# Optimization experiments

Hardware: AMD Instinct MI355X
Metric: run time of the kernel (lower is better)

The kernel has to match this reference:

```python
import jax, jax.numpy as jnp
import numpy as np

B, S, T = 8, 128, 24          # batch, src_len, max_len (enc_len = 2*S)
V, E, H = 32000, 512, 512     # vocab, embed_dim, hidden_dim
D = 3 * H + E                 # pointer-head feature dim = 2*dec_hid + emb + enc_hid


def setup_inputs() -> dict:
    key = jax.random.key(0)
    ks = jax.random.split(key, 25)
    def u(k, shape, scale):
        return jax.random.uniform(k, shape, jnp.float32, -scale, scale)
    s_h = 1.0 / np.sqrt(H).astype(np.float32)
    s_d = 1.0 / np.sqrt(D).astype(np.float32)
    s_2h = 1.0 / np.sqrt(2 * H).astype(np.float32)
    return {
        'pre_seq': jax.random.randint(ks[0], (B, S), 0, V),
        'post_seq': jax.random.randint(ks[1], (B, S), 0, V),
        'trg': jax.random.randint(ks[2], (B, T), 0, V),
        'emb': jax.random.normal(ks[3], (V, E), jnp.float32) * 0.02,
        'Wih_pre': u(ks[4], (3 * H, E), s_h), 'Whh_pre': u(ks[5], (3 * H, H), s_h),
        'bih_pre': u(ks[6], (3 * H,), s_h), 'bhh_pre': u(ks[7], (3 * H,), s_h),
        'Wih_post': u(ks[8], (3 * H, E), s_h), 'Whh_post': u(ks[9], (3 * H, H), s_h),
        'bih_post': u(ks[10], (3 * H,), s_h), 'bhh_post': u(ks[11], (3 * H,), s_h),
        'fc_enc_W': u(ks[12], (H, 2 * H), s_2h), 'fc_enc_b': u(ks[13], (H,), s_2h),
        'attn_W': u(ks[14], (H, 2 * H), s_2h), 'attn_b': u(ks[15], (H,), s_2h),
        'attn_v': u(ks[16], (1, H), s_h),
        'Wih_dec': u(ks[17], (3 * H, H + E), s_h), 'Whh_dec': u(ks[18], (3 * H, H), s_h),
        'bih_dec': u(ks[19], (3 * H,), s_h), 'bhh_dec': u(ks[20], (3 * H,), s_h),
        'fc_hid_W': u(ks[21], (D, D), s_d), 'fc_hid_b': u(ks[22], (D,), s_d),
        'fc_out_W': u(ks[23], (1, D), s_d), 'fc_out_b': u(ks[24], (1,), s_d),
    }


def gru_cell(x, h, Wih, Whh, bih, bhh):
    # torch GRU gate order: reset, update, new
    gi = x @ Wih.T + bih
    gh = h @ Whh.T + bhh
    ir, iz, inn = jnp.split(gi, 3, axis=-1)
    hr, hz, hn = jnp.split(gh, 3, axis=-1)
    r = jax.nn.sigmoid(ir + hr)
    z = jax.nn.sigmoid(iz + hz)
    n = jnp.tanh(inn + r * hn)
    return (1.0 - z) * n + z * h


def run_gru(x_seq, Wih, Whh, bih, bhh):
    # x_seq: [B, L, E] -> outputs [B, L, H], last hidden [B, H]
    h0 = jnp.zeros((x_seq.shape[0], Whh.shape[1]), x_seq.dtype)
    def step(h, x):
        h2 = gru_cell(x, h, Wih, Whh, bih, bhh)
        return h2, h2
    h_last, ys = jax.lax.scan(step, h0, jnp.swapaxes(x_seq, 0, 1))
    return jnp.swapaxes(ys, 0, 1), h_last


def reference(pre_seq, post_seq, trg, emb,
              Wih_pre, Whh_pre, bih_pre, bhh_pre,
              Wih_post, Whh_post, bih_post, bhh_post,
              fc_enc_W, fc_enc_b, attn_W, attn_b, attn_v,
              Wih_dec, Whh_dec, bih_dec, bhh_dec,
              fc_hid_W, fc_hid_b, fc_out_W, fc_out_b):
    bsz, src_len = pre_seq.shape
    # ---- Encoder (dropout in eval mode = identity) ----
    pre_out, pre_h = run_gru(emb[pre_seq], Wih_pre, Whh_pre, bih_pre, bhh_pre)
    post_out, post_h = run_gru(emb[post_seq], Wih_post, Whh_post, bih_post, bhh_post)
    enc_out = jnp.concatenate([pre_out, post_out], axis=1)          # [B, 2S, H]
    hidden = jnp.tanh(jnp.concatenate([pre_h, post_h], axis=-1) @ fc_enc_W.T + fc_enc_b)
    # ---- Attention: split attn_W into hidden- and encoder- parts (cat order: hidden, enc) ----
    W_hid, W_enc = attn_W[:, :H], attn_W[:, H:]
    enc_proj = jnp.einsum('blh,dh->bld', enc_out, W_enc) + attn_b   # step-invariant [B, L, H]
    L = enc_out.shape[1]
    # decoder input tokens: pre_seq[:, -1] then trg[:, :-1] (always teacher forced)
    tokens = jnp.concatenate([pre_seq[:, -1:], trg[:, :-1]], axis=1)  # [B, T]

    def dec_step(h, tok):
        e = emb[tok]                                                # [B, E]
        energy = jnp.tanh(enc_proj + (h @ W_hid.T)[:, None, :])     # [B, L, H]
        scores = jnp.einsum('blh,h->bl', energy, attn_v[0])
        a = jax.nn.softmax(scores, axis=1)                          # [B, L]
        weighted = jnp.einsum('bl,blh->bh', a, enc_out)             # [B, H]
        h2 = gru_cell(jnp.concatenate([e, weighted], axis=-1), h,
                      Wih_dec, Whh_dec, bih_dec, bhh_dec)           # [B, H]
        feats = jnp.concatenate([
            enc_out,
            jnp.broadcast_to(weighted[:, None, :], (bsz, L, H)),
            jnp.broadcast_to(h2[:, None, :], (bsz, L, H)),
            jnp.broadcast_to(e[:, None, :], (bsz, L, E)),
        ], axis=-1)                                                 # [B, L, 3H+E]
        hid = feats @ fc_hid_W.T + fc_hid_b                         # [B, L, D]
        logits = (hid @ fc_out_W.T + fc_out_b)[..., 0]              # [B, L]
        return h2, logits

    _, ys = jax.lax.scan(dec_step, hidden, tokens.T)                # [T, B, L]
    outs = jnp.swapaxes(ys, 0, 1)                                   # [B, T, L]
    return outs[:, :, :src_len], outs[:, :, src_len:]
```

## Files before the change

kernel.cpp:

```cpp
#include <hip/hip_runtime.h>
#include <cstdint>

#define B_ 8
#define S_ 128
#define T_ 24
#define E_ 512
#define H_ 512
#define H3_ 1536
#define L_ 256
#define D_ 2048

typedef unsigned long long u64;

__device__ __forceinline__ float fsig(float x) { return 1.0f / (1.0f + __expf(-x)); }
__device__ __forceinline__ float ftanh(float x) { return 1.0f - 2.0f / (1.0f + __expf(2.0f * x)); }
__device__ __forceinline__ float dot4(float4 a, float4 b) {
    return a.x * b.x + a.y * b.y + a.z * b.z + a.w * b.w;
}

__device__ __forceinline__ u64 cohLoadU64(const u64* p) {
    return __hip_atomic_load((u64*)p, __ATOMIC_RELAXED, __HIP_MEMORY_SCOPE_AGENT);
}
__device__ __forceinline__ void cohStoreU64(u64* p, u64 v) {
    __hip_atomic_store(p, v, __ATOMIC_RELAXED, __HIP_MEMORY_SCOPE_AGENT);
}
__device__ __forceinline__ float2 asF2(u64 v) { union { u64 u; float2 f; } x; x.u = v; return x.f; }
__device__ __forceinline__ u64 packF2(float v, float tag) { union { float2 f; u64 u; } x; x.f = make_float2(v, tag); return x.u; }

__global__ void k_init(const int* __restrict__ pre, const int* __restrict__ post,
                       const int* __restrict__ trg,
                       int* __restrict__ idxPre, int* __restrict__ idxPost,
                       int* __restrict__ idxTok, float* __restrict__ wEff) {
    int tid = blockIdx.x * 256 + threadIdx.x;
    if (tid < 1024) {
        int s = tid >> 3, b = tid & 7;
        idxPre[tid]  = pre[b * S_ + s];
        idxPost[tid] = post[b * S_ + s];
    }
    if (tid < T_ * B_) {
        int t = tid >> 3, b = tid & 7;
        idxTok[tid] = (t == 0) ? pre[b * S_ + (S_ - 1)] : trg[b * T_ + (t - 1)];
    }
    wEff[tid] = 0.f;
}

__global__ void k_clear(u64* __restrict__ p, int n) {
    int i = blockIdx.x * 256 + threadIdx.x;
    int stride = gridDim.x * 256;
    for (; i < n; i += stride) p[i] = 0ull;
}

__global__ __launch_bounds__(256) void k_gemm(
    const float* __restrict__ A, const int* __restrict__ Aidx, int lda,
    const float* __restrict__ Bm, int ldb,
    const float* __restrict__ bias, float* __restrict__ C,
    int N, int K) {
    __shared__ float As[16][68];
    __shared__ float Bs[16][68];
    const int m0 = blockIdx.x * 64, n0 = blockIdx.y * 64;
    const int tid = threadIdx.x;
    const int tm = tid >> 2;
    const int tk = (tid & 3) << 2;
    const int tx = tid & 15, ty = tid >> 4;
    const int am = m0 + tm;
    const float* Arow = A + (size_t)(Aidx ? Aidx[am] : am) * lda;
    const float* Brow = Bm + (size_t)(n0 + tm) * ldb;
    float acc[4][4] = {};
    for (int k0 = 0; k0 < K; k0 += 16) {
        float4 av = *(const float4*)(Arow + k0 + tk);
        float4 bv = *(const float4*)(Brow + k0 + tk);
        __syncthreads();
        As[tk][tm] = av.x; As[tk + 1][tm] = av.y; As[tk + 2][tm] = av.z; As[tk + 3][tm] = av.w;
        Bs[tk][tm] = bv.x; Bs[tk + 1][tm] = bv.y; Bs[tk + 2][tm] = bv.z; Bs[tk + 3][tm] = bv.w;
        __syncthreads();
#pragma unroll
        for (int k = 0; k < 16; ++k) {
            float4 a4 = *(const float4*)(&As[k][ty << 2]);
            float4 b4 = *(const float4*)(&Bs[k][tx << 2]);
            float ar[4] = {a4.x, a4.y, a4.z, a4.w};
            float br[4] = {b4.x, b4.y, b4.z, b4.w};
#pragma unroll
            for (int i = 0; i < 4; ++i)
#pragma unroll
                for (int j = 0; j < 4; ++j) acc[i][j] += ar[i] * br[j];
        }
    }
    float4 bb = bias ? *(const float4*)(bias + n0 + (tx << 2)) : make_float4(0.f, 0.f, 0.f, 0.f);
#pragma unroll
    for (int i = 0; i < 4; ++i) {
        int m = m0 + (ty << 2) + i;
        float4 o;
        o.x = acc[i][0] + bb.x; o.y = acc[i][1] + bb.y;
        o.z = acc[i][2] + bb.z; o.w = acc[i][3] + bb.w;
        *(float4*)(C + (size_t)m * N + n0 + (tx << 2)) = o;
    }
}

__global__ void k_weff(const float* __restrict__ fcW, const float* __restrict__ fcB,
                       const float* __restrict__ voW, const float* __restrict__ voB,
                       float* __restrict__ wEff, float* __restrict__ bEff) {
    __shared__ float red[256];
    int bx = blockIdx.x;
    if (bx < 128) {
        int cblk = bx & 7, q = bx >> 3;
        int col = cblk * 256 + threadIdx.x;
        int j0 = q * 128;
        float acc = 0.f;
        for (int j = j0; j < j0 + 128; ++j) acc += voW[j] * fcW[(size_t)j * D_ + col];
        atomicAdd(wEff + col, acc);
    } else {
        float p = 0.f;
        for (int j = threadIdx.x; j < D_; j += 256) p += voW[j] * fcB[j];
        red[threadIdx.x] = p;
        __syncthreads();
        for (int s = 128; s > 0; s >>= 1) {
            if (threadIdx.x < s) red[threadIdx.x] += red[threadIdx.x + s];
            __syncthreads();
        }
        if (threadIdx.x == 0) bEff[0] = red[0] + voB[0];
    }
}

__global__ __launch_bounds__(512, 2) void k_encoder(
    const float* __restrict__ giPre, const float* __restrict__ giPost,
    const float* __restrict__ WhhPre, const float* __restrict__ WhhPost,
    const float* __restrict__ bhhPre, const float* __restrict__ bhhPost,
    float* __restrict__ encOut, u64* __restrict__ encEx) {
    const int bx = blockIdx.x;
    const int chain = bx >> 4;
    const int p = bx & 15;
    const int gr = chain >> 3, b = chain & 7;
    const int kb = p << 5;
    const int tid = threadIdx.x;
    const int c = tid >> 4, l = tid & 15;
    const int j = kb + c;
    const float* gi  = gr ? giPost : giPre;
    const float* Whh = gr ? WhhPost : WhhPre;
    const float* bhh = gr ? bhhPost : bhhPre;
    u64* ex0 = encEx + chain * 512;

    __shared__ float hS[576];

    float wr[32], wz[32], wn[32];
    {
        const float* r0 = Whh + (size_t)j * 512 + l * 32;
        const float* r1 = r0 + 512 * 512;
        const float* r2 = r1 + 512 * 512;
#pragma unroll
        for (int m = 0; m < 32; ++m) { wr[m] = r0[m]; wz[m] = r1[m]; wn[m] = r2[m]; }
    }
    const float bh0 = bhh[j], bh1 = bhh[512 + j], bh2 = bhh[1024 + j];

    for (int t = 0; t < S_; ++t) {
        float g0 = 0.f, g1 = 0.f, g2 = 0.f;
        if (l == 0) {
            size_t gb = ((size_t)(t << 3) + b) * H3_;
            g0 = gi[gb + j]; g1 = gi[gb + 512 + j]; g2 = gi[gb + 1024 + j];
        }
        if (t == 0) {
            hS[(tid >> 5) * 36 + (tid & 31)] = 0.f;
        } else {
            const float tag = (float)t;
            const u64* src = ex0 + (t & 1) * 8192;
            float v;
            for (;;) {
                float2 f = asF2(cohLoadU64(src + tid));
                if (f.y == tag) { v = f.x; break; }
                __builtin_amdgcn_s_sleep(1);
            }
            hS[(tid >> 5) * 36 + (tid & 31)] = v;
        }
        __syncthreads();
        const float* hseg = hS + l * 36;
        float a0 = 0.f, a1 = 0.f, a2 = 0.f;
#pragma unroll
        for (int m = 0; m < 32; ++m) {
            float hv = hseg[m];
            a0 += wr[m] * hv; a1 += wz[m] * hv; a2 += wn[m] * hv;
        }
#pragma unroll
        for (int off = 8; off; off >>= 1) {
            a0 += __shfl_xor(a0, off, 16);
            a1 += __shfl_xor(a1, off, 16);
            a2 += __shfl_xor(a2, off, 16);
        }
        if (l == 0) {
            float r = fsig(g0 + a0 + bh0);
            float z = fsig(g1 + a1 + bh1);
            float n = ftanh(g2 + r * (a2 + bh2));
            float h2 = (1.f - z) * n + z * hS[p * 36 + c];
            cohStoreU64(ex0 + ((t + 1) & 1) * 8192 + j, packF2(h2, (float)(t + 1)));
            encOut[(((size_t)(b << 8) + (gr << 7) + t) << 9) + j] = h2;
        }
        __syncthreads();
    }
}

__global__ void k_fcenc(const float* __restrict__ encOut, const float* __restrict__ W,
                        const float* __restrict__ bias, float* __restrict__ h) {
    int o = blockIdx.x * 256 + threadIdx.x;
    int b = o >> 9, j = o & 511;
    const float4* w4 = (const float4*)(W + (size_t)j * 1024);
    const float4* pre4 = (const float4*)(encOut + (((size_t)(b << 8) + 127) << 9));
    const float4* post4 = (const float4*)(encOut + (((size_t)(b << 8) + 255) << 9));
    float acc = bias[j];
    for (int k = 0; k < 128; ++k) acc += dot4(w4[k], pre4[k]);
    for (int k = 0; k < 128; ++k) acc += dot4(w4[128 + k], post4[k]);
    h[o] = ftanh(acc);
}

__global__ void k_encdot(const float* __restrict__ encOut, const float* __restrict__ wEff,
                         float* __restrict__ encDot) {
    int wid = threadIdx.x >> 6, lane = threadIdx.x & 63;
    int gw = blockIdx.x * 4 + wid;
    for (int o = gw; o < 2048; o += 128) {
        const float* row = encOut + ((size_t)o << 9);
        float s = 0.f;
        for (int k = lane; k < 512; k += 64) s += row[k] * wEff[k];
        for (int off = 32; off; off >>= 1) s += __shfl_down(s, off);
        if (lane == 0) encDot[o] = s;
    }
}

__global__ void k_edot4(const float* __restrict__ emb, const int* __restrict__ idxTok,
                        const float* __restrict__ wEff, float* __restrict__ eDot4) {
    int o = blockIdx.x;
    int lane = threadIdx.x;
    const float* row = emb + (size_t)idxTok[o] * E_;
    const float* w = wEff + 1536;
    float s = 0.f;
    for (int k = lane; k < 512; k += 64) s += row[k] * w[k];
    for (int off = 32; off; off >>= 1) s += __shfl_down(s, off);
    if (lane == 0) eDot4[o] = s;
}

__global__ __launch_bounds__(512, 2) void k_decoder(
    const float* __restrict__ encOut, const float* __restrict__ encProj,
    const float* __restrict__ attnW, const float* __restrict__ attnV,
    const float* __restrict__ WihDec, const float* __restrict__ WhhDec,
    const float* __restrict__ bhhDec, const float* __restrict__ giE,
    const float* __restrict__ wEff, const float* __restrict__ hBuf,
    u64* __restrict__ hEx, u64* __restrict__ hpEx,
    u64* __restrict__ scEx, u64* __restrict__ wtEx,
    float* __restrict__ cpart) {
    const int tid = threadIdx.x;
    const int bx = blockIdx.x;
    __shared__ float hL[4096];
    __shared__ float xL[4096];
    __shared__ float mS[1408];

    if (bx < 32) {
        const int g = bx;
        const int s = tid >> 5, kq = tid & 31;
        const int j = (g << 4) + s;
        float wr[16], wz[16], wn[16], vr[16], vz[16], vn[16];
#pragma unroll
        for (int m = 0; m < 16; ++m) {
            int k = kq + 32 * m;
            wr[m] = WhhDec[(size_t)j * 512 + k];
            wz[m] = WhhDec[(size_t)(512 + j) * 512 + k];
            wn[m] = WhhDec[(size_t)(1024 + j) * 512 + k];
            vr[m] = WihDec[(size_t)j * 1024 + 512 + k];
            vz[m] = WihDec[(size_t)(512 + j) * 1024 + 512 + k];
            vn[m] = WihDec[(size_t)(1024 + j) * 1024 + 512 + k];
        }
        if (tid < 48) mS[1152 + tid] = bhhDec[(tid >> 4) * 512 + (g << 4) + (tid & 15)];
        __syncthreads();
        for (int t = 0; t < T_; ++t) {
            if (t == 0) {
#pragma unroll
                for (int i = 0; i < 8; ++i) hL[tid + 512 * i] = hBuf[tid + 512 * i];
            } else {
                const float tagh = (float)t;
                const u64* src = hEx + (t & 1) * 4096;
                float v[8];
                for (;;) {
                    u64 rr[8];
#pragma unroll
                    for (int i = 0; i < 8; ++i) rr[i] = cohLoadU64(src + tid + 512 * i);
                    bool ok = true;
#pragma unroll
                    for (int i = 0; i < 8; ++i) { float2 f = asF2(rr[i]); v[i] = f.x; ok &= (f.y == tagh); }
                    if (ok) break;
                    __builtin_amdgcn_s_sleep(1);
                }
#pragma unroll
                for (int i = 0; i < 8; ++i) hL[tid + 512 * i] = v[i];
            }
            __syncthreads();
            for (int b = 0; b < 8; ++b) {
                const float* hb = hL + (b << 9);
                float ar = 0.f, az = 0.f, an = 0.f;
#pragma unroll
                for (int m = 0; m < 16; ++m) {
                    float hv = hb[kq + 32 * m];
                    ar += wr[m] * hv; az += wz[m] * hv; an += wn[m] * hv;
                }
#pragma unroll
                for (int off = 16; off; off >>= 1) {
                    ar += __shfl_xor(ar, off); az += __shfl_xor(az, off); an += __shfl_xor(an, off);
                }
                if (kq == 0) {
                    mS[s * 8 + b]       = ar + mS[1152 + s];
                    mS[128 + s * 8 + b] = az + mS[1168 + s];
                    mS[256 + s * 8 + b] = an + mS[1184 + s];
                }
            }
            if (tid < 384) {
                int b = tid / 48, idx = tid % 48, g3 = idx >> 4, ss = idx & 15;
                mS[768 + g3 * 128 + ss * 8 + b] =
                    giE[((size_t)(t << 3) + b) * H3_ + g3 * 512 + (g << 4) + ss];
            }
            {
                const float tagw = (float)(t + 1);
                const u64* src = wtEx + (t & 1) * 4096;
                float v[8];
                for (;;) {
                    u64 rr[8];
#pragma unroll
                    for (int i = 0; i < 8; ++i) rr[i] = cohLoadU64(src + tid + 512 * i);
                    bool ok = true;
#pragma unroll
                    for (int i = 0; i < 8; ++i) { float2 f = asF2(rr[i]); v[i] = f.x; ok &= (f.y == tagw); }
                    if (ok) break;
                    __builtin_amdgcn_s_sleep(1);
                }
#pragma unroll
                for (int i = 0; i < 8; ++i) xL[tid + 512 * i] = v[i];
            }
            __syncthreads();
            for (int b = 0; b < 8; ++b) {
                const float* wb = xL + (b << 9);
                float ar = 0.f, az = 0.f, an = 0.f;
#pragma unroll
                for (int m = 0; m < 16; ++m) {
                    float wv = wb[kq + 32 * m];
                    ar += vr[m] * wv; az += vz[m] * wv; an += vn[m] * wv;
                }
#pragma unroll
                for (int off = 16; off; off >>= 1) {
                    ar += __shfl_xor(ar, off); az += __shfl_xor(az, off); an += __shfl_xor(an, off);
                }
                if (kq == 0) {
                    mS[384 + s * 8 + b] = ar;
                    mS[512 + s * 8 + b] = az;
                    mS[640 + s * 8 + b] = an;
                }
            }
            __syncthreads();
            if (tid < 128) {
                int ss = tid >> 3, b = tid & 7;
                int jj = (g << 4) + ss;
                int o = ss * 8 + b;
                float ghr = mS[o], ghz = mS[128 + o], ghn = mS[256 + o];
                float gir = mS[384 + o] + mS[768 + o];
                float giz = mS[512 + o] + mS[896 + o];
                float gin = mS[640 + o] + mS[1024 + o];
                float r = fsig(gir + ghr), z = fsig(giz + ghz);
                float n = ftanh(gin + r * ghn);
                float h2 = (1.f - z) * n + z * hL[(b << 9) + jj];
                cohStoreU64(hEx + ((t + 1) & 1) * 4096 + (b << 9) + jj, packF2(h2, (float)(t + 1)));
                mS[1200 + o] = h2 * wEff[1024 + jj];
            }
            __syncthreads();
            if (tid < 8) {
                float pc = 0.f;
#pragma unroll
                for (int q = 0; q < 16; ++q) pc += mS[1200 + q * 8 + tid];
                cpart[(tid * T_ + t) * 48 + g] = pc;
            }
            __syncthreads();
        }
    } else if (bx < 48) {
        const int w = bx - 32;
        const int s = tid >> 5, kq = tid & 31;
        const int r0 = (w << 5) + s, r1 = r0 + 16;
        float wa[16], wb[16];
#pragma unroll
        for (int m = 0; m < 16; ++m) {
            int k = kq + 32 * m;
            wa[m] = attnW[(size_t)r0 * 1024 + k];
            wb[m] = attnW[(size_t)r1 * 1024 + k];
        }
        for (int t = 0; t < T_; ++t) {
            if (t == 0) {
#pragma unroll
                for (int i = 0; i < 8; ++i) hL[tid + 512 * i] = hBuf[tid + 512 * i];
            } else {
                const float tagh = (float)t;
                const u64* src = hEx + (t & 1) * 4096;
                float v[8];
                for (;;) {
                    u64 rr[8];
#pragma unroll
                    for (int i = 0; i < 8; ++i) rr[i] = cohLoadU64(src + tid + 512 * i);
                    bool ok = true;
#pragma unroll
                    for (int i = 0; i < 8; ++i) { float2 f = asF2(rr[i]); v[i] = f.x; ok &= (f.y == tagh); }
                    if (ok) break;
                    __builtin_amdgcn_s_sleep(1);
                }
#pragma unroll
                for (int i = 0; i < 8; ++i) hL[tid + 512 * i] = v[i];
            }
            __syncthreads();
            const float tago = (float)(t + 1);
            u64* dst = hpEx + (t & 1) * 4096;
            for (int b = 0; b < 8; ++b) {
                const float* hb = hL + (b << 9);
                float aa = 0.f, ab = 0.f;
#pragma unroll
                for (int m = 0; m < 16; ++m) {
                    float hv = hb[kq + 32 * m];
                    aa += wa[m] * hv; ab += wb[m] * hv;
                }
#pragma unroll
                for (int off = 16; off; off >>= 1) { aa += __shfl_xor(aa, off); ab += __shfl_xor(ab, off); }
                if (kq == 0) {
                    cohStoreU64(dst + (b << 9) + r0, packF2(aa, tago));
                    cohStoreU64(dst + (b << 9) + r1, packF2(ab, tago));
                }
            }
            __syncthreads();
        }
    } else if (bx < 112) {
        const int id = bx - 48;
        const int b = id >> 3, lq = id & 7;
        const int kq = tid & 63, lg = tid >> 6;
        for (int t = 0; t < T_; ++t) {
            const float tagi = (float)(t + 1);
            {
                const u64* src = hpEx + (t & 1) * 4096 + (b << 9);
                float2 f;
                for (;;) {
                    f = asF2(cohLoadU64(src + tid));
                    if (f.y == tagi) break;
                    __builtin_amdgcn_s_sleep(1);
                }
                hL[tid] = f.x;
            }
            __syncthreads();
            u64* dst = scEx + (t & 1) * 2048 + (b << 8);
#pragma unroll
            for (int i = 0; i < 4; ++i) {
                int l = (lq << 5) + lg + (i << 3);
                const float* ep = encProj + (((size_t)(b << 8) + l) << 9);
                float sc = 0.f;
#pragma unroll
                for (int m = 0; m < 8; ++m) {
                    int k = kq + (m << 6);
                    sc += attnV[k] * ftanh(ep[k] + hL[k]);
                }
#pragma unroll
                for (int off = 32; off; off >>= 1) sc += __shfl_xor(sc, off);
                if (kq == 0) cohStoreU64(dst + l, packF2(sc, tagi));
            }
            __syncthreads();
        }
    } else if (bx < 176) {
        const int id = bx - 112;
        const int b = id >> 3, cq = id & 7;
        const int c = tid & 63, lg = tid >> 6;
        for (int t = 0; t < T_; ++t) {
            const float tagi = (float)(t + 1);
            if (tid < 256) {
                const u64* src = scEx + (t & 1) * 2048 + (b << 8);
                float2 f;
                for (;;) {
                    f = asF2(cohLoadU64(src + tid));
                    if (f.y == tagi) break;
                    __builtin_amdgcn_s_sleep(1);
                }
                mS[tid] = f.x;
            }
            __syncthreads();
            if (tid < 256) mS[256 + tid] = mS[tid];
            __syncthreads();
            for (int st = 128; st; st >>= 1) {
                if (tid < st) mS[256 + tid] = fmaxf(mS[256 + tid], mS[256 + tid + st]);
                __syncthreads();
            }
            float mx = mS[256];
            __syncthreads();
            if (tid < 256) { float ex = __expf(mS[tid] - mx); mS[tid] = ex; mS[256 + tid] = ex; }
            __syncthreads();
            for (int st = 128; st; st >>= 1) {
                if (tid < st) mS[256 + tid] += mS[256 + tid + st];
                __syncthreads();
            }
            float inv = 1.f / mS[256];
            float acc = 0.f;
            const float* eb = encOut + (((size_t)(b << 8)) << 9) + (cq << 6) + c;
#pragma unroll
            for (int m = 0; m < 32; ++m) {
                int l = lg + (m << 3);
                acc += mS[l] * eb[(size_t)l << 9];
            }
            mS[512 + lg * 64 + c] = acc;
            __syncthreads();
            if (tid < 64) {
                float wv = 0.f;
#pragma unroll
                for (int q = 0; q < 8; ++q) wv += mS[512 + q * 64 + tid];
                wv *= inv;
                cohStoreU64(wtEx + (t & 1) * 4096 + (b << 9) + (cq << 6) + tid, packF2(wv, tagi));
                mS[1024 + tid] = wv * wEff[512 + (cq << 6) + tid];
            }
            __syncthreads();
            if (tid == 0) {
                float pc = 0.f;
                for (int q = 0; q < 64; ++q) pc += mS[1024 + q];
                cpart[(b * T_ + t) * 48 + 32 + cq] = pc;
            }
            __syncthreads();
        }
    }
}

__global__ void k_csum(const float* __restrict__ cpart, const float* __restrict__ eDot4,
                       const float* __restrict__ bEff, float* __restrict__ cBuf) {
    int tid = threadIdx.x;
    if (tid < 192) {
        int b = tid / 24, t = tid % 24;
        float acc = eDot4[t * 8 + b] + bEff[0];
        const float* p = cpart + (b * T_ + t) * 48;
#pragma unroll
        for (int k = 0; k < 40; ++k) acc += p[k];
        cBuf[b * T_ + t] = acc;
    }
}

__global__ void k_final(const float* __restrict__ encDot, const float* __restrict__ c,
                        float* __restrict__ out) {
    int idx = blockIdx.x * 256 + threadIdx.x;
    const int half = B_ * T_ * S_;
    int w = idx < half ? idx : idx - half;
    int b = w / (T_ * S_);
    int r = w % (T_ * S_);
    int t = r / S_, sidx = r % S_;
    int l = (idx < half) ? sidx : (S_ + sidx);
    out[idx] = encDot[b * L_ + l] + c[b * T_ + t];
}

extern "C" void kernel_launch(void* const* d_in, const int* in_sizes, int n_in,
                              void* d_out, int out_size, void* d_ws, size_t ws_size,
                              hipStream_t stream) {
    const int* pre = (const int*)d_in[0];
    const int* post = (const int*)d_in[1];
    const int* trg = (const int*)d_in[2];
    const float* emb = (const float*)d_in[3];
    const float* WihPre = (const float*)d_in[4];
    const float* WhhPre = (const float*)d_in[5];
    const float* bihPre = (const float*)d_in[6];
    const float* bhhPre = (const float*)d_in[7];
    const float* WihPost = (const float*)d_in[8];
    const float* WhhPost = (const float*)d_in[9];
    const float* bihPost = (const float*)d_in[10];
    const float* bhhPost = (const float*)d_in[11];
    const float* fcEncW = (const float*)d_in[12];
    const float* fcEncB = (const float*)d_in[13];
    const float* attnW = (const float*)d_in[14];
    const float* attnB = (const float*)d_in[15];
    const float* attnV = (const float*)d_in[16];
    const float* WihDec = (const float*)d_in[17];
    const float* WhhDec = (const float*)d_in[18];
    const float* bihDec = (const float*)d_in[19];
    const float* bhhDec = (const float*)d_in[20];
    const float* fcHidW = (const float*)d_in[21];
    const float* fcHidB = (const float*)d_in[22];
    const float* fcOutW = (const float*)d_in[23];
    const float* fcOutB = (const float*)d_in[24];
    float* outp = (float*)d_out;

    float* base = (float*)d_ws;
    size_t off = 0;
    auto alloc = [&](size_t n) {
        float* p = base + off;
        off += (n + 63) & ~(size_t)63;
        return p;
    };
    float* giPre = alloc(1024 * 1536);
    float* giPost = alloc(1024 * 1536);
    float* giE = alloc(192 * 1536);
    float* encOut = alloc(8 * 256 * 512);
    float* encProj = alloc(8 * 256 * 512);
    float* wEff = alloc(2048);
    float* bEff = alloc(64);
    float* encDot = alloc(2048);
    float* eDot4 = alloc(256);
    float* hBuf = alloc(4096);
    float* cBuf = alloc(256);
    float* encExF = alloc(32768);
    float* hExF = alloc(16384);
    float* hpExF = alloc(16384);
    float* scExF = alloc(8192);
    float* wtExF = alloc(16384);
    float* cpart = alloc(8 * 24 * 48);
    int* idxPre = (int*)alloc(1024);
    int* idxPost = (int*)alloc(1024);
    int* idxTok = (int*)alloc(256);

    k_init<<<8, 256, 0, stream>>>(pre, post, trg, idxPre, idxPost, idxTok, wEff);
    k_clear<<<512, 256, 0, stream>>>((u64*)encExF, 45056);
    k_weff<<<129, 256, 0, stream>>>(fcHidW, fcHidB, fcOutW, fcOutB, wEff, bEff);
    k_gemm<<<dim3(16, 24), 256, 0, stream>>>(emb, idxPre, 512, WihPre, 512, bihPre, giPre, 1536, 512);
    k_gemm<<<dim3(16, 24), 256, 0, stream>>>(emb, idxPost, 512, WihPost, 512, bihPost, giPost, 1536, 512);
    k_gemm<<<dim3(3, 24), 256, 0, stream>>>(emb, idxTok, 512, WihDec, 1024, bihDec, giE, 1536, 512);
    k_encoder<<<256, 512, 0, stream>>>(giPre, giPost, WhhPre, WhhPost, bhhPre, bhhPost,
                                       encOut, (u64*)encExF);
    k_gemm<<<dim3(32, 8), 256, 0, stream>>>(encOut, nullptr, 512, attnW + 512, 1024, attnB, encProj, 512, 512);
    k_fcenc<<<16, 256, 0, stream>>>(encOut, fcEncW, fcEncB, hBuf);
    k_encdot<<<32, 256, 0, stream>>>(encOut, wEff, encDot);
    k_edot4<<<192, 64, 0, stream>>>(emb, idxTok, wEff, eDot4);
    k_decoder<<<176, 512, 0, stream>>>(encOut, encProj, attnW, attnV, WihDec, WhhDec, bhhDec,
                                       giE, wEff, hBuf, (u64*)hExF, (u64*)hpExF,
                                       (u64*)scExF, (u64*)wtExF, cpart);
    k_csum<<<1, 256, 0, stream>>>(cpart, eDot4, bEff, cBuf);
    k_final<<<192, 256, 0, stream>>>(encDot, cBuf, outp);
}
```

Before: 1.023 ms.

## Fuse encoder input projection into recurrence and merge auxiliary kernels

Drops the separate pre/post input-projection GEMMs and has each encoder block hold both Wih and Whh slices in registers, computing the input gate contribution per step from gathered embeddings. The small setup kernels (init, clear, weff, gemms, fc_enc) are merged into a boot kernel and a multi-role mid kernel, and encdot/edot4 become extra blocks of the decoder. The decoder is also reorganised: it precomputes hidden attention projections into a larger exchange buffer and uses wave-level shuffle reductions for the softmax. The goal is fewer launches and less GEMM time off the critical path, at the cost of doubled register pressure and extra per-step work in the serial encoder loop.

```diff
diff --git a/kernel.cpp b/kernel.cpp
--- a/kernel.cpp
+++ b/kernel.cpp
@@ -27,37 +27,33 @@
 __device__ __forceinline__ float2 asF2(u64 v) { union { u64 u; float2 f; } x; x.u = v; return x.f; }
 __device__ __forceinline__ u64 packF2(float v, float tag) { union { float2 f; u64 u; } x; x.f = make_float2(v, tag); return x.u; }
 
-__global__ void k_init(const int* __restrict__ pre, const int* __restrict__ post,
+__global__ void k_boot(const int* __restrict__ pre, const int* __restrict__ post,
                        const int* __restrict__ trg,
                        int* __restrict__ idxPre, int* __restrict__ idxPost,
-                       int* __restrict__ idxTok, float* __restrict__ wEff) {
-    int tid = blockIdx.x * 256 + threadIdx.x;
-    if (tid < 1024) {
-        int s = tid >> 3, b = tid & 7;
-        idxPre[tid]  = pre[b * S_ + s];
-        idxPost[tid] = post[b * S_ + s];
-    }
-    if (tid < T_ * B_) {
-        int t = tid >> 3, b = tid & 7;
-        idxTok[tid] = (t == 0) ? pre[b * S_ + (S_ - 1)] : trg[b * T_ + (t - 1)];
-    }
-    wEff[tid] = 0.f;
-}
-
-__global__ void k_clear(u64* __restrict__ p, int n) {
-    int i = blockIdx.x * 256 + threadIdx.x;
-    int stride = gridDim.x * 256;
-    for (; i < n; i += stride) p[i] = 0ull;
-}
-
-__global__ __launch_bounds__(256) void k_gemm(
+                       int* __restrict__ idxTok, float* __restrict__ wEff,
+                       u64* __restrict__ clr, int n) {
+    int gtid = blockIdx.x * 256 + threadIdx.x;
+    for (int i = gtid; i < n; i += gridDim.x * 256) clr[i] = 0ull;
+    if (gtid < 1024) {
+        int s = gtid >> 3, b = gtid & 7;
+        idxPre[gtid]  = pre[b * S_ + s];
+        idxPost[gtid] = post[b * S_ + s];
+    }
+    if (gtid < T_ * B_) {
+        int t = gtid >> 3, b = gtid & 7;
+        idxTok[gtid] = (t == 0) ? pre[b * S_ + (S_ - 1)] : trg[b * T_ + (t - 1)];
+    }
+    if (gtid < 2048) wEff[gtid] = 0.f;
+}
+
+__device__ void gemm_body(
     const float* __restrict__ A, const int* __restrict__ Aidx, int lda,
     const float* __restrict__ Bm, int ldb,
     const float* __restrict__ bias, float* __restrict__ C,
-    int N, int K) {
+    int N, int K, int gbx, int gby) {
     __shared__ float As[16][68];
     __shared__ float Bs[16][68];
-    const int m0 = blockIdx.x * 64, n0 = blockIdx.y * 64;
+    const int m0 = gbx * 64, n0 = gby * 64;
     const int tid = threadIdx.x;
     const int tm = tid >> 2;
     const int tk = (tid & 3) << 2;
@@ -96,33 +92,61 @@
     }
 }
 
-__global__ void k_weff(const float* __restrict__ fcW, const float* __restrict__ fcB,
-                       const float* __restrict__ voW, const float* __restrict__ voB,
-                       float* __restrict__ wEff, float* __restrict__ bEff) {
-    __shared__ float red[256];
-    int bx = blockIdx.x;
-    if (bx < 128) {
-        int cblk = bx & 7, q = bx >> 3;
-        int col = cblk * 256 + threadIdx.x;
-        int j0 = q * 128;
-        float acc = 0.f;
-        for (int j = j0; j < j0 + 128; ++j) acc += voW[j] * fcW[(size_t)j * D_ + col];
-        atomicAdd(wEff + col, acc);
+__global__ __launch_bounds__(256) void k_mid(
+    const float* __restrict__ emb, const int* __restrict__ idxTok,
+    const float* __restrict__ WihDec, const float* __restrict__ bihDec, float* __restrict__ giE,
+    const float* __restrict__ encOut, const float* __restrict__ attnW,
+    const float* __restrict__ attnB, float* __restrict__ encProj,
+    const float* __restrict__ fcHidW, const float* __restrict__ fcHidB,
+    const float* __restrict__ fcOutW, const float* __restrict__ fcOutB,
+    float* __restrict__ wEff, float* __restrict__ bEff,
+    const float* __restrict__ fcEncW, const float* __restrict__ fcEncB,
+    float* __restrict__ hBuf) {
+    const int bx = blockIdx.x;
+    const int tid = threadIdx.x;
+    if (bx < 72) {
+        gemm_body(emb, idxTok, 512, WihDec, 1024, bihDec, giE, 1536, 512, bx % 3, bx / 3);
+    } else if (bx < 328) {
+        int r = bx - 72;
+        gemm_body(encOut, nullptr, 512, attnW + 512, 1024, attnB, encProj, 512, 512, r & 31, r >> 5);
+    } else if (bx < 457) {
+        __shared__ float red[256];
+        int wb = bx - 328;
+        if (wb < 128) {
+            int cblk = wb & 7, q = wb >> 3;
+            int col = cblk * 256 + tid;
+            int j0 = q * 128;
+            float acc = 0.f;
+            for (int j = j0; j < j0 + 128; ++j) acc += fcOutW[j] * fcHidW[(size_t)j * D_ + col];
+            atomicAdd(wEff + col, acc);
+        } else {
+            float p = 0.f;
+            for (int j = tid; j < D_; j += 256) p += fcOutW[j] * fcHidB[j];
+            red[tid] = p;
+            __syncthreads();
+            for (int s = 128; s > 0; s >>= 1) {
+                if (tid < s) red[tid] += red[tid + s];
+                __syncthreads();
+            }
+            if (tid == 0) bEff[0] = red[0] + fcOutB[0];
+        }
     } else {
-        float p = 0.f;
-        for (int j = threadIdx.x; j < D_; j += 256) p += voW[j] * fcB[j];
-        red[threadIdx.x] = p;
-        __syncthreads();
-        for (int s = 128; s > 0; s >>= 1) {
-            if (threadIdx.x < s) red[threadIdx.x] += red[threadIdx.x + s];
-            __syncthreads();
-        }
-        if (threadIdx.x == 0) bEff[0] = red[0] + voB[0];
+        int o = (bx - 457) * 256 + tid;
+        int b = o >> 9, j = o & 511;
+        const float4* w4 = (const float4*)(fcEncW + (size_t)j * 1024);
+        const float4* pre4 = (const float4*)(encOut + (((size_t)(b << 8) + 127) << 9));
+        const float4* post4 = (const float4*)(encOut + (((size_t)(b << 8) + 255) << 9));
+        float acc = fcEncB[j];
+        for (int k = 0; k < 128; ++k) acc += dot4(w4[k], pre4[k]);
+        for (int k = 0; k < 128; ++k) acc += dot4(w4[128 + k], post4[k]);
+        hBuf[o] = ftanh(acc);
     }
 }
 
 __global__ __launch_bounds__(512, 2) void k_encoder(
-    const float* __restrict__ giPre, const float* __restrict__ giPost,
+    const float* __restrict__ emb, const int* __restrict__ idxPre, const int* __restrict__ idxPost,
+    const float* __restrict__ WihPre, const float* __restrict__ WihPost,
+    const float* __restrict__ bihPre, const float* __restrict__ bihPost,
     const float* __restrict__ WhhPre, const float* __restrict__ WhhPost,
     const float* __restrict__ bhhPre, const float* __restrict__ bhhPost,
     float* __restrict__ encOut, u64* __restrict__ encEx) {
@@ -134,29 +158,38 @@
     const int tid = threadIdx.x;
     const int c = tid >> 4, l = tid & 15;
     const int j = kb + c;
-    const float* gi  = gr ? giPost : giPre;
+    const float* Wih = gr ? WihPost : WihPre;
+    const float* bih = gr ? bihPost : bihPre;
     const float* Whh = gr ? WhhPost : WhhPre;
     const float* bhh = gr ? bhhPost : bhhPre;
+    const int* idx = gr ? idxPost : idxPre;
     u64* ex0 = encEx + chain * 512;
 
     __shared__ float hS[576];
-
-    float wr[32], wz[32], wn[32];
+    __shared__ float eS[576];
+
+    float wr[32], wz[32], wn[32], ur[32], uz[32], un[32];
     {
         const float* r0 = Whh + (size_t)j * 512 + l * 32;
         const float* r1 = r0 + 512 * 512;
         const float* r2 = r1 + 512 * 512;
-#pragma unroll
-        for (int m = 0; m < 32; ++m) { wr[m] = r0[m]; wz[m] = r1[m]; wn[m] = r2[m]; }
-    }
-    const float bh0 = bhh[j], bh1 = bhh[512 + j], bh2 = bhh[1024 + j];
+        const float* u0 = Wih + (size_t)j * 512 + l * 32;
+        const float* u1 = u0 + 512 * 512;
+        const float* u2 = u1 + 512 * 512;
+#pragma unroll
+        for (int m = 0; m < 32; ++m) {
+            wr[m] = r0[m]; wz[m] = r1[m]; wn[m] = r2[m];
+            ur[m] = u0[m]; uz[m] = u1[m]; un[m] = u2[m];
+        }
+    }
+    const float b0 = bih[j] + bhh[j];
+    const float b1 = bih[512 + j] + bhh[512 + j];
+    const float bi2 = bih[1024 + j];
+    const float bh2 = bhh[1024 + j];
 
     for (int t = 0; t < S_; ++t) {
-        float g0 = 0.f, g1 = 0.f, g2 = 0.f;
-        if (l == 0) {
-            size_t gb = ((size_t)(t << 3) + b) * H3_;
-            g0 = gi[gb + j]; g1 = gi[gb + 512 + j]; g2 = gi[gb + 1024 + j];
-        }
+        int tok = idx[t * 8 + b];
+        float ev = emb[(size_t)tok * 512 + tid];
         if (t == 0) {
             hS[(tid >> 5) * 36 + (tid & 31)] = 0.f;
         } else {
@@ -170,68 +203,36 @@
             }
             hS[(tid >> 5) * 36 + (tid & 31)] = v;
         }
+        eS[(tid >> 5) * 36 + (tid & 31)] = ev;
         __syncthreads();
         const float* hseg = hS + l * 36;
-        float a0 = 0.f, a1 = 0.f, a2 = 0.f;
+        const float* eseg = eS + l * 36;
+        float a0 = 0.f, a1 = 0.f, a2h = 0.f, a2i = 0.f;
 #pragma unroll
         for (int m = 0; m < 32; ++m) {
-            float hv = hseg[m];
-            a0 += wr[m] * hv; a1 += wz[m] * hv; a2 += wn[m] * hv;
+            float hv = hseg[m], evv = eseg[m];
+            a0 += wr[m] * hv + ur[m] * evv;
+            a1 += wz[m] * hv + uz[m] * evv;
+            a2h += wn[m] * hv;
+            a2i += un[m] * evv;
         }
 #pragma unroll
         for (int off = 8; off; off >>= 1) {
             a0 += __shfl_xor(a0, off, 16);
             a1 += __shfl_xor(a1, off, 16);
-            a2 += __shfl_xor(a2, off, 16);
+            a2h += __shfl_xor(a2h, off, 16);
+            a2i += __shfl_xor(a2i, off, 16);
         }
         if (l == 0) {
-            float r = fsig(g0 + a0 + bh0);
-            float z = fsig(g1 + a1 + bh1);
-            float n = ftanh(g2 + r * (a2 + bh2));
+            float r = fsig(a0 + b0);
+            float z = fsig(a1 + b1);
+            float n = ftanh(a2i + bi2 + r * (a2h + bh2));
             float h2 = (1.f - z) * n + z * hS[p * 36 + c];
             cohStoreU64(ex0 + ((t + 1) & 1) * 8192 + j, packF2(h2, (float)(t + 1)));
             encOut[(((size_t)(b << 8) + (gr << 7) + t) << 9) + j] = h2;
         }
         __syncthreads();
     }
-}
-
-__global__ void k_fcenc(const float* __restrict__ encOut, const float* __restrict__ W,
-                        const float* __restrict__ bias, float* __restrict__ h) {
-    int o = blockIdx.x * 256 + threadIdx.x;
-    int b = o >> 9, j = o & 511;
-    const float4* w4 = (const float4*)(W + (size_t)j * 1024);
-    const float4* pre4 = (const float4*)(encOut + (((size_t)(b << 8) + 127) << 9));
-    const float4* post4 = (const float4*)(encOut + (((size_t)(b << 8) + 255) << 9));
-    float acc = bias[j];
-    for (int k = 0; k < 128; ++k) acc += dot4(w4[k], pre4[k]);
-    for (int k = 0; k < 128; ++k) acc += dot4(w4[128 + k], post4[k]);
-    h[o] = ftanh(acc);
-}
-
-__global__ void k_encdot(const float* __restrict__ encOut, const float* __restrict__ wEff,
-                         float* __restrict__ encDot) {
-    int wid = threadIdx.x >> 6, lane = threadIdx.x & 63;
-    int gw = blockIdx.x * 4 + wid;
-    for (int o = gw; o < 2048; o += 128) {
-        const float* row = encOut + ((size_t)o << 9);
-        float s = 0.f;
-        for (int k = lane; k < 512; k += 64) s += row[k] * wEff[k];
-        for (int off = 32; off; off >>= 1) s += __shfl_down(s, off);
-        if (lane == 0) encDot[o] = s;
-    }
-}
-
-__global__ void k_edot4(const float* __restrict__ emb, const int* __restrict__ idxTok,
-                        const float* __restrict__ wEff, float* __restrict__ eDot4) {
-    int o = blockIdx.x;
-    int lane = threadIdx.x;
-    const float* row = emb + (size_t)idxTok[o] * E_;
-    const float* w = wEff + 1536;
-    float s = 0.f;
-    for (int k = lane; k < 512; k += 64) s += row[k] * w[k];
-    for (int off = 32; off; off >>= 1) s += __shfl_down(s, off);
-    if (lane == 0) eDot4[o] = s;
 }
 
 __global__ __launch_bounds__(512, 2) void k_decoder(
@@ -240,20 +241,19 @@
     const float* __restrict__ WihDec, const float* __restrict__ WhhDec,
     const float* __restrict__ bhhDec, const float* __restrict__ giE,
     const float* __restrict__ wEff, const float* __restrict__ hBuf,
-    u64* __restrict__ hEx, u64* __restrict__ hpEx,
+    const float* __restrict__ emb, const int* __restrict__ idxTok,
+    u64* __restrict__ hEx, u64* __restrict__ hpP,
     u64* __restrict__ scEx, u64* __restrict__ wtEx,
-    float* __restrict__ cpart) {
+    float* __restrict__ cpart, float* __restrict__ encDot, float* __restrict__ eDot4) {
     const int tid = threadIdx.x;
     const int bx = blockIdx.x;
-    __shared__ float hL[4096];
-    __shared__ float xL[4096];
-    __shared__ float mS[1408];
+    __shared__ float shm[9664];
 
     if (bx < 32) {
         const int g = bx;
         const int s = tid >> 5, kq = tid & 31;
         const int j = (g << 4) + s;
-        float wr[16], wz[16], wn[16], vr[16], vz[16], vn[16];
+        float wr[16], wz[16], wn[16], vr[16], vz[16], vn[16], ap[16];
 #pragma unroll
         for (int m = 0; m < 16; ++m) {
             int k = kq + 32 * m;
@@ -263,22 +263,38 @@
             vr[m] = WihDec[(size_t)j * 1024 + 512 + k];
             vz[m] = WihDec[(size_t)(512 + j) * 1024 + 512 + k];
             vn[m] = WihDec[(size_t)(1024 + j) * 1024 + 512 + k];
-        }
-        if (tid < 48) mS[1152 + tid] = bhhDec[(tid >> 4) * 512 + (g << 4) + (tid & 15)];
+            ap[m] = attnW[(size_t)tid * 1024 + (g << 4) + m];
+        }
+        float* hL = shm;
+        float* xL = shm + 4096;
+        float* mS = shm + 8192;
+        if (tid < 128) { int ss = tid >> 3, bb = tid & 7; mS[1152 + tid] = hBuf[(bb << 9) + (g << 4) + ss]; }
+        if (tid < 48) mS[1280 + tid] = bhhDec[(tid >> 4) * 512 + (g << 4) + (tid & 15)];
         __syncthreads();
+        {
+            u64* hdst = hpP + (size_t)g * 4096;
+#pragma unroll
+            for (int bb = 0; bb < 8; ++bb) {
+                float acch = 0.f;
+#pragma unroll
+                for (int m = 0; m < 16; ++m) acch += ap[m] * mS[1152 + m * 8 + bb];
+                cohStoreU64(hdst + bb * 512 + tid, packF2(acch, 1.0f));
+            }
+        }
         for (int t = 0; t < T_; ++t) {
+            const int par = t & 1;
+            const float tagi = (float)(t + 1);
             if (t == 0) {
 #pragma unroll
                 for (int i = 0; i < 8; ++i) hL[tid + 512 * i] = hBuf[tid + 512 * i];
             } else {
                 const float tagh = (float)t;
-                const u64* src = hEx + (t & 1) * 4096;
+                const u64* src = hEx + par * 4096;
                 float v[8];
                 for (;;) {
-                    u64 rr[8];
+                    u64 rr[8]; bool ok = true;
 #pragma unroll
                     for (int i = 0; i < 8; ++i) rr[i] = cohLoadU64(src + tid + 512 * i);
-                    bool ok = true;
 #pragma unroll
                     for (int i = 0; i < 8; ++i) { float2 f = asF2(rr[i]); v[i] = f.x; ok &= (f.y == tagh); }
                     if (ok) break;
@@ -288,8 +304,8 @@
                 for (int i = 0; i < 8; ++i) hL[tid + 512 * i] = v[i];
             }
             __syncthreads();
-            for (int b = 0; b < 8; ++b) {
-                const float* hb = hL + (b << 9);
+            for (int bb = 0; bb < 8; ++bb) {
+                const float* hb = hL + (bb << 9);
                 float ar = 0.f, az = 0.f, an = 0.f;
 #pragma unroll
                 for (int m = 0; m < 16; ++m) {
@@ -301,27 +317,25 @@
                     ar += __shfl_xor(ar, off); az += __shfl_xor(az, off); an += __shfl_xor(an, off);
                 }
                 if (kq == 0) {
-                    mS[s * 8 + b]       = ar + mS[1152 + s];
-                    mS[128 + s * 8 + b] = az + mS[1168 + s];
-                    mS[256 + s * 8 + b] = an + mS[1184 + s];
+                    mS[s * 8 + bb]       = ar;
+                    mS[128 + s * 8 + bb] = az;
+                    mS[256 + s * 8 + bb] = an;
                 }
             }
             if (tid < 384) {
-                int b = tid / 48, idx = tid % 48, g3 = idx >> 4, ss = idx & 15;
-                mS[768 + g3 * 128 + ss * 8 + b] =
-                    giE[((size_t)(t << 3) + b) * H3_ + g3 * 512 + (g << 4) + ss];
+                int bb = tid / 48, idx2 = tid % 48, g3 = idx2 >> 4, ss = idx2 & 15;
+                mS[768 + g3 * 128 + ss * 8 + bb] =
+                    giE[((size_t)(t << 3) + bb) * H3_ + g3 * 512 + (g << 4) + ss];
             }
             {
-                const float tagw = (float)(t + 1);
-                const u64* src = wtEx + (t & 1) * 4096;
+                const u64* src = wtEx + par * 4096;
                 float v[8];
                 for (;;) {
-                    u64 rr[8];
+                    u64 rr[8]; bool ok = true;
 #pragma unroll
                     for (int i = 0; i < 8; ++i) rr[i] = cohLoadU64(src + tid + 512 * i);
-                    bool ok = true;
-#pragma unroll
-                    for (int i = 0; i < 8; ++i) { float2 f = asF2(rr[i]); v[i] = f.x; ok &= (f.y == tagw); }
+#pragma unroll
+                    for (int i = 0; i < 8; ++i) { float2 f = asF2(rr[i]); v[i] = f.x; ok &= (f.y == tagi); }
                     if (ok) break;
                     __builtin_amdgcn_s_sleep(1);
                 }
@@ -329,8 +343,8 @@
                 for (int i = 0; i < 8; ++i) xL[tid + 512 * i] = v[i];
             }
             __syncthreads();
-            for (int b = 0; b < 8; ++b) {
-                const float* wb = xL + (b << 9);
+            for (int bb = 0; bb < 8; ++bb) {
+                const float* wb = xL + (bb << 9);
                 float ar = 0.f, az = 0.f, an = 0.f;
 #pragma unroll
                 for (int m = 0; m < 16; ++m) {
@@ -342,178 +356,175 @@
                     ar += __shfl_xor(ar, off); az += __shfl_xor(az, off); an += __shfl_xor(an, off);
                 }
                 if (kq == 0) {
-                    mS[384 + s * 8 + b] = ar;
-                    mS[512 + s * 8 + b] = az;
-                    mS[640 + s * 8 + b] = an;
+                    mS[384 + s * 8 + bb] = ar;
+                    mS[512 + s * 8 + bb] = az;
+                    mS[640 + s * 8 + bb] = an;
                 }
             }
             __syncthreads();
             if (tid < 128) {
-                int ss = tid >> 3, b = tid & 7;
+                int ss = tid >> 3, bb = tid & 7;
                 int jj = (g << 4) + ss;
-                int o = ss * 8 + b;
-                float ghr = mS[o], ghz = mS[128 + o], ghn = mS[256 + o];
+                int o = ss * 8 + bb;
+                float ghr = mS[o]       + mS[1280 + ss];
+                float ghz = mS[128 + o] + mS[1296 + ss];
+                float ghn = mS[256 + o] + mS[1312 + ss];
                 float gir = mS[384 + o] + mS[768 + o];
                 float giz = mS[512 + o] + mS[896 + o];
                 float gin = mS[640 + o] + mS[1024 + o];
                 float r = fsig(gir + ghr), z = fsig(giz + ghz);
                 float n = ftanh(gin + r * ghn);
-                float h2 = (1.f - z) * n + z * hL[(b << 9) + jj];
-                cohStoreU64(hEx + ((t + 1) & 1) * 4096 + (b << 9) + jj, packF2(h2, (float)(t + 1)));
-                mS[1200 + o] = h2 * wEff[1024 + jj];
+                float h2 = (1.f - z) * n + z * hL[(bb << 9) + jj];
+                cohStoreU64(hEx + ((t + 1) & 1) * 4096 + (bb << 9) + jj, packF2(h2, (float)(t + 1)));
+                mS[1152 + o] = h2;
+                mS[1328 + o] = h2 * wEff[1024 + jj];
             }
             __syncthreads();
             if (tid < 8) {
                 float pc = 0.f;
 #pragma unroll
-                for (int q = 0; q < 16; ++q) pc += mS[1200 + q * 8 + tid];
+                for (int q = 0; q < 16; ++q) pc += mS[1328 + q * 8 + tid];
                 cpart[(tid * T_ + t) * 48 + g] = pc;
             }
-            __syncthreads();
-        }
-    } else if (bx < 48) {
-        const int w = bx - 32;
-        const int s = tid >> 5, kq = tid & 31;
-        const int r0 = (w << 5) + s, r1 = r0 + 16;
-        float wa[16], wb[16];
-#pragma unroll
-        for (int m = 0; m < 16; ++m) {
-            int k = kq + 32 * m;
-            wa[m] = attnW[(size_t)r0 * 1024 + k];
-            wb[m] = attnW[(size_t)r1 * 1024 + k];
-        }
-        for (int t = 0; t < T_; ++t) {
-            if (t == 0) {
-#pragma unroll
-                for (int i = 0; i < 8; ++i) hL[tid + 512 * i] = hBuf[tid + 512 * i];
-            } else {
-                const float tagh = (float)t;
-                const u64* src = hEx + (t & 1) * 4096;
-                float v[8];
-                for (;;) {
-                    u64 rr[8];
-#pragma unroll
-                    for (int i = 0; i < 8; ++i) rr[i] = cohLoadU64(src + tid + 512 * i);
-                    bool ok = true;
-#pragma unroll
-                    for (int i = 0; i < 8; ++i) { float2 f = asF2(rr[i]); v[i] = f.x; ok &= (f.y == tagh); }
-                    if (ok) break;
-                    __builtin_amdgcn_s_sleep(1);
-                }
-#pragma unroll
-                for (int i = 0; i < 8; ++i) hL[tid + 512 * i] = v[i];
-            }
-            __syncthreads();
-            const float tago = (float)(t + 1);
-            u64* dst = hpEx + (t & 1) * 4096;
-            for (int b = 0; b < 8; ++b) {
-                const float* hb = hL + (b << 9);
-                float aa = 0.f, ab = 0.f;
-#pragma unroll
-                for (int m = 0; m < 16; ++m) {
-                    float hv = hb[kq + 32 * m];
-                    aa += wa[m] * hv; ab += wb[m] * hv;
-                }
-#pragma unroll
-                for (int off = 16; off; off >>= 1) { aa += __shfl_xor(aa, off); ab += __shfl_xor(ab, off); }
-                if (kq == 0) {
-                    cohStoreU64(dst + (b << 9) + r0, packF2(aa, tago));
-                    cohStoreU64(dst + (b << 9) + r1, packF2(ab, tago));
-                }
-            }
-            __syncthreads();
-        }
-    } else if (bx < 112) {
-        const int id = bx - 48;
+            if (t < T_ - 1) {
+                const float tg = (float)(t + 2);
+                u64* hdst = hpP + (size_t)((t + 1) & 1) * 131072 + (size_t)g * 4096;
+#pragma unroll
+                for (int bb = 0; bb < 8; ++bb) {
+                    float acch = 0.f;
+#pragma unroll
+                    for (int m = 0; m < 16; ++m) acch += ap[m] * mS[1152 + m * 8 + bb];
+                    cohStoreU64(hdst + bb * 512 + tid, packF2(acch, tg));
+                }
+            }
+            __syncthreads();
+        }
+    } else if (bx < 96) {
+        const int id = bx - 32;
         const int b = id >> 3, lq = id & 7;
+        float* hpS = shm;
+        float* vS  = shm + 512;
+        vS[tid] = attnV[tid];
+        __syncthreads();
         const int kq = tid & 63, lg = tid >> 6;
         for (int t = 0; t < T_; ++t) {
+            const int par = t & 1;
             const float tagi = (float)(t + 1);
             {
-                const u64* src = hpEx + (t & 1) * 4096 + (b << 9);
-                float2 f;
+                const u64* src = hpP + (size_t)par * 131072 + (size_t)b * 512 + tid;
+                float sum;
                 for (;;) {
-                    f = asF2(cohLoadU64(src + tid));
-                    if (f.y == tagi) break;
-                    __builtin_amdgcn_s_sleep(1);
-                }
-                hL[tid] = f.x;
-            }
-            __syncthreads();
-            u64* dst = scEx + (t & 1) * 2048 + (b << 8);
+                    bool ok = true; float s2 = 0.f;
+                    u64 ra[16];
+#pragma unroll
+                    for (int pp = 0; pp < 16; ++pp) ra[pp] = cohLoadU64(src + (size_t)pp * 4096);
+#pragma unroll
+                    for (int pp = 0; pp < 16; ++pp) { float2 f = asF2(ra[pp]); s2 += f.x; ok &= (f.y == tagi); }
+#pragma unroll
+                    for (int pp = 0; pp < 16; ++pp) ra[pp] = cohLoadU64(src + (size_t)(16 + pp) * 4096);
+#pragma unroll
+                    for (int pp = 0; pp < 16; ++pp) { float2 f = asF2(ra[pp]); s2 += f.x; ok &= (f.y == tagi); }
+                    if (ok) { sum = s2; break; }
+                    __builtin_amdgcn_s_sleep(2);
+                }
+                hpS[tid] = sum;
+            }
+            __syncthreads();
+            u64* dst = scEx + par * 2048 + (b << 8);
 #pragma unroll
             for (int i = 0; i < 4; ++i) {
-                int l = (lq << 5) + lg + (i << 3);
-                const float* ep = encProj + (((size_t)(b << 8) + l) << 9);
+                int ll = lg + (i << 3);
+                const float* ep = encProj + (((size_t)(b << 8) + (lq << 5) + ll) << 9);
                 float sc = 0.f;
 #pragma unroll
                 for (int m = 0; m < 8; ++m) {
                     int k = kq + (m << 6);
-                    sc += attnV[k] * ftanh(ep[k] + hL[k]);
+                    sc += vS[k] * ftanh(ep[k] + hpS[k]);
                 }
 #pragma unroll
                 for (int off = 32; off; off >>= 1) sc += __shfl_xor(sc, off);
-                if (kq == 0) cohStoreU64(dst + l, packF2(sc, tagi));
-            }
-            __syncthreads();
-        }
-    } else if (bx < 176) {
-        const int id = bx - 112;
+                if (kq == 0) cohStoreU64(dst + (lq << 5) + ll, packF2(sc, tagi));
+            }
+            __syncthreads();
+        }
+    } else if (bx < 160) {
+        const int id = bx - 96;
         const int b = id >> 3, cq = id & 7;
         const int c = tid & 63, lg = tid >> 6;
+        float* aS = shm;
+        float* rS = shm + 256;
+        float* wS = shm + 288;
+        float* lp = shm + 800;
         for (int t = 0; t < T_; ++t) {
+            const int par = t & 1;
             const float tagi = (float)(t + 1);
+            float sc = 0.f;
             if (tid < 256) {
-                const u64* src = scEx + (t & 1) * 2048 + (b << 8);
-                float2 f;
+                const u64* src = scEx + par * 2048 + (b << 8) + tid;
                 for (;;) {
-                    f = asF2(cohLoadU64(src + tid));
-                    if (f.y == tagi) break;
+                    float2 f = asF2(cohLoadU64(src));
+                    if (f.y == tagi) { sc = f.x; break; }
                     __builtin_amdgcn_s_sleep(1);
                 }
-                mS[tid] = f.x;
-            }
-            __syncthreads();
-            if (tid < 256) mS[256 + tid] = mS[tid];
-            __syncthreads();
-            for (int st = 128; st; st >>= 1) {
-                if (tid < st) mS[256 + tid] = fmaxf(mS[256 + tid], mS[256 + tid + st]);
-                __syncthreads();
-            }
-            float mx = mS[256];
-            __syncthreads();
-            if (tid < 256) { float ex = __expf(mS[tid] - mx); mS[tid] = ex; mS[256 + tid] = ex; }
-            __syncthreads();
-            for (int st = 128; st; st >>= 1) {
-                if (tid < st) mS[256 + tid] += mS[256 + tid + st];
-                __syncthreads();
-            }
-            float inv = 1.f / mS[256];
+            }
+            float m = (tid < 256) ? sc : -1e30f;
+#pragma unroll
+            for (int off = 32; off; off >>= 1) m = fmaxf(m, __shfl_xor(m, off));
+            if ((tid & 63) == 0) rS[tid >> 6] = m;
+            __syncthreads();
+            float mx = fmaxf(fmaxf(rS[0], rS[1]), fmaxf(rS[2], rS[3]));
+            float e = (tid < 256) ? __expf(sc - mx) : 0.f;
+            float ssum = e;
+#pragma unroll
+            for (int off = 32; off; off >>= 1) ssum += __shfl_xor(ssum, off);
+            if ((tid & 63) == 0) rS[8 + (tid >> 6)] = ssum;
+            if (tid < 256) aS[tid] = e;
+            __syncthreads();
+            float inv = 1.f / (rS[8] + rS[9] + rS[10] + rS[11]);
             float acc = 0.f;
-            const float* eb = encOut + (((size_t)(b << 8)) << 9) + (cq << 6) + c;
-#pragma unroll
-            for (int m = 0; m < 32; ++m) {
-                int l = lg + (m << 3);
-                acc += mS[l] * eb[(size_t)l << 9];
-            }
-            mS[512 + lg * 64 + c] = acc;
+#pragma unroll
+            for (int mm = 0; mm < 32; ++mm) {
+                int l = lg + (mm << 3);
+                acc += aS[l] * encOut[(((size_t)(b << 8) + l) << 9) + (cq << 6) + c];
+            }
+            wS[lg * 64 + c] = acc;
             __syncthreads();
             if (tid < 64) {
                 float wv = 0.f;
 #pragma unroll
-                for (int q = 0; q < 8; ++q) wv += mS[512 + q * 64 + tid];
+                for (int q = 0; q < 8; ++q) wv += wS[q * 64 + tid];
                 wv *= inv;
-                cohStoreU64(wtEx + (t & 1) * 4096 + (b << 9) + (cq << 6) + tid, packF2(wv, tagi));
-                mS[1024 + tid] = wv * wEff[512 + (cq << 6) + tid];
+                cohStoreU64(wtEx + par * 4096 + (b << 9) + (cq << 6) + tid, packF2(wv, tagi));
+                lp[tid] = wv * wEff[512 + (cq << 6) + tid];
             }
             __syncthreads();
             if (tid == 0) {
                 float pc = 0.f;
-                for (int q = 0; q < 64; ++q) pc += mS[1024 + q];
+                for (int q = 0; q < 64; ++q) pc += lp[q];
                 cpart[(b * T_ + t) * 48 + 32 + cq] = pc;
             }
             __syncthreads();
         }
+    } else if (bx < 164) {
+        int wid = tid >> 6, lane = tid & 63;
+        int gw = (bx - 160) * 8 + wid;
+        for (int o = gw; o < 2048; o += 32) {
+            const float* row = encOut + ((size_t)o << 9);
+            float s = 0.f;
+            for (int k = lane; k < 512; k += 64) s += row[k] * wEff[k];
+            for (int off = 32; off; off >>= 1) s += __shfl_down(s, off);
+            if (lane == 0) encDot[o] = s;
+        }
+    } else {
+        int wg = bx - 164;
+        int o = wg * 8 + (tid >> 6);
+        int lane = tid & 63;
+        const float* row = emb + (size_t)idxTok[o] * E_;
+        const float* w = wEff + 1536;
+        float s = 0.f;
+        for (int k = lane; k < 512; k += 64) s += row[k] * w[k];
+        for (int off = 32; off; off >>= 1) s += __shfl_down(s, off);
+        if (lane == 0) eDot4[o] = s;
     }
 }
 
@@ -579,8 +590,6 @@
         off += (n + 63) & ~(size_t)63;
         return p;
     };
-    float* giPre = alloc(1024 * 1536);
-    float* giPost = alloc(1024 * 1536);
     float* giE = alloc(192 * 1536);
     float* encOut = alloc(8 * 256 * 512);
     float* encProj = alloc(8 * 256 * 512);
@@ -591,8 +600,8 @@
     float* hBuf = alloc(4096);
     float* cBuf = alloc(256);
     float* encExF = alloc(32768);
-    float* hExF = alloc(16384);
-    float* hpExF = alloc(16384);
+    float* hExF  = alloc(16384);
+    float* hpPF  = alloc(524288);
     float* scExF = alloc(8192);
     float* wtExF = alloc(16384);
     float* cpart = alloc(8 * 24 * 48);
@@ -600,21 +609,21 @@
     int* idxPost = (int*)alloc(1024);
     int* idxTok = (int*)alloc(256);
 
-    k_init<<<8, 256, 0, stream>>>(pre, post, trg, idxPre, idxPost, idxTok, wEff);
-    k_clear<<<512, 256, 0, stream>>>((u64*)encExF, 45056);
-    k_weff<<<129, 256, 0, stream>>>(fcHidW, fcHidB, fcOutW, fcOutB, wEff, bEff);
-    k_gemm<<<dim3(16, 24), 256, 0, stream>>>(emb, idxPre, 512, WihPre, 512, bihPre, giPre, 1536, 512);
-    k_gemm<<<dim3(16, 24), 256, 0, stream>>>(emb, idxPost, 512, WihPost, 512, bihPost, giPost, 1536, 512);
-    k_gemm<<<dim3(3, 24), 256, 0, stream>>>(emb, idxTok, 512, WihDec, 1024, bihDec, giE, 1536, 512);
-    k_encoder<<<256, 512, 0, stream>>>(giPre, giPost, WhhPre, WhhPost, bhhPre, bhhPost,
-                                       encOut, (u64*)encExF);
-    k_gemm<<<dim3(32, 8), 256, 0, stream>>>(encOut, nullptr, 512, attnW + 512, 1024, attnB, encProj, 512, 512);
-    k_fcenc<<<16, 256, 0, stream>>>(encOut, fcEncW, fcEncB, hBuf);
-    k_encdot<<<32, 256, 0, stream>>>(encOut, wEff, encDot);
-    k_edot4<<<192, 64, 0, stream>>>(emb, idxTok, wEff, eDot4);
-    k_decoder<<<176, 512, 0, stream>>>(encOut, encProj, attnW, attnV, WihDec, WhhDec, bhhDec,
-                                       giE, wEff, hBuf, (u64*)hExF, (u64*)hpExF,
-                                       (u64*)scExF, (u64*)wtExF, cpart);
+    const int clearN = (32768 + 16384 + 524288 + 8192 + 16384) / 2;
+    k_boot<<<512, 256, 0, stream>>>(pre, post, trg, idxPre, idxPost, idxTok, wEff,
+                                    (u64*)encExF, clearN);
+    k_encoder<<<256, 512, 0, stream>>>(emb, idxPre, idxPost, WihPre, WihPost,
+                                       bihPre, bihPost, WhhPre, WhhPost,
+                                       bhhPre, bhhPost, encOut, (u64*)encExF);
+    k_mid<<<473, 256, 0, stream>>>(emb, idxTok, WihDec, bihDec, giE,
+                                   encOut, attnW, attnB, encProj,
+                                   fcHidW, fcHidB, fcOutW, fcOutB, wEff, bEff,
+                                   fcEncW, fcEncB, hBuf);
+    k_decoder<<<188, 512, 0, stream>>>(encOut, encProj, attnW, attnV,
+                                       WihDec, WhhDec, bhhDec, giE, wEff, hBuf,
+                                       emb, idxTok,
+                                       (u64*)hExF, (u64*)hpPF, (u64*)scExF, (u64*)wtExF,
+                                       cpart, encDot, eDot4);
     k_csum<<<1, 256, 0, stream>>>(cpart, eDot4, bEff, cBuf);
     k_final<<<192, 256, 0, stream>>>(encDot, cBuf, outp);
 }
```

Measured after the change: 902.2 us. 1.13x faster.
